# Performance work log

Hardware: AMD Instinct MI355X
Metric: run time of the kernel (lower is better)

## Reference

```python
import jax, jax.numpy as jnp
import numpy as np

EPS = 1e-5

def _layernorm(x, g, b):
    # LayerNorm over last dim (head_dim), eps=1e-5 like nn.LayerNorm
    mu = jnp.mean(x, axis=-1, keepdims=True)
    var = jnp.mean(jnp.square(x - mu), axis=-1, keepdims=True)
    return (x - mu) * jax.lax.rsqrt(var + EPS) * g + b

def _rotate_half(x):
    d = x.shape[-1] // 2
    return jnp.concatenate([-x[..., d:], x[..., :d]], axis=-1)

def _apply_rotary(x, cos, sin):
    # x: [B,S,H,D]; cos/sin: [S,D] broadcast over batch and heads
    c = cos[None, :, None, :]
    s = sin[None, :, None, :]
    return x * c + _rotate_half(x) * s

def setup_inputs() -> dict:
    key = jax.random.key(0)
    ks = jax.random.split(key, 16)
    B, S, Dm = 2, 1024, 2048
    H, Hkv, Dh = 16, 4, 128
    f = lambda k, shp: (jax.random.normal(k, shp, dtype=jnp.float32) * 0.02)
    return {
        "hidden_states": jax.random.normal(ks[0], (B, S, Dm), dtype=jnp.float32),
        "cos": jax.random.uniform(ks[1], (S, Dh), dtype=jnp.float32),
        "sin": jax.random.uniform(ks[2], (S, Dh), dtype=jnp.float32),
        "Wq": f(ks[3], (H * Dh, Dm)),   "bq": jnp.zeros((H * Dh,), jnp.float32),
        "Wk": f(ks[4], (Hkv * Dh, Dm)), "bk": jnp.zeros((Hkv * Dh,), jnp.float32),
        "Wv": f(ks[5], (Hkv * Dh, Dm)), "bv": jnp.zeros((Hkv * Dh,), jnp.float32),
        "Wo": f(ks[6], (Dm, H * Dh)),   "bo": jnp.zeros((Dm,), jnp.float32),
        "qn_g": jnp.ones((Dh,), jnp.float32), "qn_b": jnp.zeros((Dh,), jnp.float32),
        "kn_g": jnp.ones((Dh,), jnp.float32), "kn_b": jnp.zeros((Dh,), jnp.float32),
        "cu_seqlens": jnp.array([0, S, 2 * S], dtype=jnp.int32),
        "max_s": 1024,
    }

def reference(hidden_states, cos, sin, Wq, bq, Wk, bk, Wv, bv, Wo, bo,
              qn_g, qn_b, kn_g, kn_b, cu_seqlens, max_s):
    B, S, Dm = hidden_states.shape
    Dh = qn_g.shape[0]
    H = Wq.shape[0] // Dh
    Hkv = Wk.shape[0] // Dh
    scale = 1.0 / jnp.sqrt(jnp.float32(Dh))

    q = (hidden_states @ Wq.T + bq).reshape(B, S, H, Dh)
    k = (hidden_states @ Wk.T + bk).reshape(B, S, Hkv, Dh)
    v = (hidden_states @ Wv.T + bv).reshape(B, S, Hkv, Dh)

    q = _apply_rotary(_layernorm(q, qn_g, qn_b), cos, sin)
    k = _apply_rotary(_layernorm(k, kn_g, kn_b), cos, sin)

    # GQA: repeat_interleave kv heads to match q heads
    n_rep = H // Hkv
    if n_rep > 1:
        k = jnp.repeat(k, n_rep, axis=2)
        v = jnp.repeat(v, n_rep, axis=2)

    # scores: [B,H,S,S]
    scores = jnp.einsum('bqhd,bkhd->bhqk', q, k) * scale
    causal = jnp.tril(jnp.ones((S, S), dtype=bool))
    scores = jnp.where(causal[None, None], scores, jnp.finfo(scores.dtype).min)
    weights = jax.nn.softmax(scores, axis=-1)
    out = jnp.einsum('bhqk,bkhd->bqhd', weights, v).reshape(B, S, H * Dh)
    return out @ Wo.T + bo
```

## Files before the change

kernel.cpp:

```cpp
#include <hip/hip_runtime.h>
#include <cmath>

typedef __attribute__((ext_vector_type(8))) short bf16x8;
typedef __attribute__((ext_vector_type(4))) short s16x4;
typedef __attribute__((ext_vector_type(4))) float f32x4;

#define MFMA_BF16 __builtin_amdgcn_mfma_f32_16x16x32_bf16

__device__ __forceinline__ float bf2f(short s) {
    unsigned u = ((unsigned)(unsigned short)s) << 16;
    return __builtin_bit_cast(float, u);
}
__device__ __forceinline__ short f2bf(float f) {
    unsigned u = __builtin_bit_cast(unsigned, f);
    u += 0x7fffu + ((u >> 16) & 1u);
    return (short)(u >> 16);
}

__device__ __forceinline__ void gl_lds16(const short* gp, short* lp) {
    __builtin_amdgcn_global_load_lds(
        (const __attribute__((address_space(1))) unsigned int*)gp,
        (__attribute__((address_space(3))) unsigned int*)lp, 16, 0, 0);
}

__global__ __launch_bounds__(256) void cvt5(
    const float* s0, short* d0, int n0,
    const float* s1, short* d1, int n1,
    const float* s2, short* d2, int n2,
    const float* s3, short* d3, int n3,
    const float* s4, short* d4, int n4)
{
    long long i = (long long)blockIdx.x * 1024 + threadIdx.x * 4;
    const float* s; short* d;
    if      (i < n0)                  { s = s0; d = d0; }
    else if ((i -= n0) < n1)          { s = s1; d = d1; }
    else if ((i -= n1) < n2)          { s = s2; d = d2; }
    else if ((i -= n2) < n3)          { s = s3; d = d3; }
    else      { i -= n3;                s = s4; d = d4; }
    float4 v = *(const float4*)(s + i);
    s16x4 o;
    o[0] = f2bf(v.x); o[1] = f2bf(v.y); o[2] = f2bf(v.z); o[3] = f2bf(v.w);
    *(s16x4*)(d + i) = o;
}

template <int MODE>
__global__ __launch_bounds__(256) void gemm_t(
    const short* __restrict__ A, const short* __restrict__ W,
    const float* __restrict__ bq, const float* __restrict__ bk,
    const float* __restrict__ bv,
    short* __restrict__ qo, short* __restrict__ ko, short* __restrict__ vo,
    float* __restrict__ fo,
    int M, int K, int S, int Hkv, int Nq, int Nkv, int N)
{
    __shared__ __align__(16) short As[2][8 * 512];
    __shared__ __align__(16) short Bs[2][4 * 512];

    const int w    = threadIdx.x >> 6;
    const int lane = threadIdx.x & 63;
    const int l15  = lane & 15;
    const int quad = lane >> 4;
    const int wy   = w >> 1;
    const int wx   = w & 1;

    unsigned gx = gridDim.x, gy = gridDim.y;
    unsigned bx = blockIdx.x, by = blockIdx.y;
    if ((gx & 3) == 0 && (gy & 1) == 0) {
        unsigned lin = by * gx + bx;
        unsigned xcd = lin & 7, idx = lin >> 3;
        unsigned n   = gx >> 2;
        bx = (xcd & 3) * n + idx % n;
        by = (xcd >> 2) * (gy >> 1) + idx / n;
    }
    const int m0 = by * 128;
    const int n0 = bx * 64;

    const short* Ab = A + (size_t)m0 * K;
    const short* Wb = W + (size_t)n0 * K;

    const int srow = lane >> 2;
    const int scol = ((lane & 3) ^ ((srow >> 1) & 3)) * 8;
    auto stage = [&](int buf, int kofs) {
#pragma unroll
        for (int i = 0; i < 2; i++) {
            const int c = 2 * w + i;
            gl_lds16(Ab + (size_t)(c * 16 + srow) * K + kofs + scol,
                     As[buf] + c * 512 + lane * 8);
        }
        gl_lds16(Wb + (size_t)(w * 16 + srow) * K + kofs + scol,
                 Bs[buf] + w * 512 + lane * 8);
    };

    f32x4 acc[4][2];
#pragma unroll
    for (int i = 0; i < 4; i++)
#pragma unroll
        for (int j = 0; j < 2; j++) acc[i][j] = f32x4{0.f, 0.f, 0.f, 0.f};

    const int ridx = (l15 * 4 + (quad ^ ((l15 >> 1) & 3))) * 8;
    const int nk = K / 32;
    stage(0, 0);
    __syncthreads();

    for (int kt = 0; kt < nk; kt++) {
        const int cur = kt & 1;
        if (kt + 1 < nk) stage(cur ^ 1, (kt + 1) * 32);

        bf16x8 af[4], bfr[2];
#pragma unroll
        for (int i = 0; i < 4; i++)
            af[i] = *(const bf16x8*)(As[cur] + (wy * 4 + i) * 512 + ridx);
#pragma unroll
        for (int j = 0; j < 2; j++)
            bfr[j] = *(const bf16x8*)(Bs[cur] + (wx * 2 + j) * 512 + ridx);
#pragma unroll
        for (int i = 0; i < 4; i++)
#pragma unroll
            for (int j = 0; j < 2; j++)
                acc[i][j] = MFMA_BF16(af[i], bfr[j], acc[i][j], 0, 0, 0);
        __syncthreads();
    }

#pragma unroll
    for (int i = 0; i < 4; i++) {
#pragma unroll
        for (int j = 0; j < 2; j++) {
            const int col = n0 + wx * 32 + j * 16 + l15;
#pragma unroll
            for (int r = 0; r < 4; r++) {
                const int row = m0 + wy * 64 + i * 16 + quad * 4 + r;
                float v = acc[i][j][r];
                if constexpr (MODE == 0) {
                    if (col < Nq) {
                        qo[(size_t)row * Nq + col] = f2bf(v + bq[col]);
                    } else if (col < Nq + Nkv) {
                        int cn = col - Nq;
                        ko[(size_t)row * Nkv + cn] = f2bf(v + bk[cn]);
                    } else {
                        int cn = col - Nq - Nkv;
                        int b  = row / S, s = row - b * S;
                        int hk = cn >> 7, dh = cn & 127;
                        vo[(size_t)((b * Hkv + hk) * 128 + dh) * S + s] = f2bf(v + bv[cn]);
                    }
                } else {
                    fo[(size_t)row * N + col] = v + bq[col];
                }
            }
        }
    }
}

__global__ __launch_bounds__(256) void ln_rope2(
    const short* __restrict__ Xq, short* __restrict__ Yq,
    const short* __restrict__ Xk, short* __restrict__ Yk,
    const float* __restrict__ qg, const float* __restrict__ qbe,
    const float* __restrict__ kg, const float* __restrict__ kbe,
    const float* __restrict__ cosp, const float* __restrict__ sinp,
    int H, int Hkv, int S, int nq)
{
    int gw = blockIdx.x * 4 + (threadIdx.x >> 6);
    const int lane = threadIdx.x & 63;
    const short* X; short* Y; const float* g; const float* bt; int Hc;
    if (gw < nq) { X = Xq; Y = Yq; g = qg; bt = qbe; Hc = H; }
    else { gw -= nq; X = Xk; Y = Yk; g = kg; bt = kbe; Hc = Hkv; }

    const int h  = gw % Hc;
    const int rs = gw / Hc;
    const int b  = rs / S;
    const int s  = rs - b * S;

    const short* x = X + ((size_t)rs * Hc + h) * 128;
    float x0 = bf2f(x[lane]), x1 = bf2f(x[lane + 64]);

    float sum = x0 + x1;
    float sq  = x0 * x0 + x1 * x1;
#pragma unroll
    for (int off = 32; off > 0; off >>= 1) {
        sum += __shfl_xor(sum, off, 64);
        sq  += __shfl_xor(sq, off, 64);
    }
    float mu  = sum * (1.f / 128.f);
    float var = sq * (1.f / 128.f) - mu * mu;
    float rinv = rsqrtf(var + 1e-5f);

    float y0 = (x0 - mu) * rinv * g[lane]      + bt[lane];
    float y1 = (x1 - mu) * rinv * g[lane + 64] + bt[lane + 64];

    float c0 = cosp[(size_t)s * 128 + lane];
    float c1 = cosp[(size_t)s * 128 + lane + 64];
    float s0 = sinp[(size_t)s * 128 + lane];
    float s1 = sinp[(size_t)s * 128 + lane + 64];

    float o0 = y0 * c0 - y1 * s0;
    float o1 = y1 * c1 + y0 * s1;

    short* yp = Y + ((size_t)(b * Hc + h) * S + s) * 128;
    yp[lane]      = f2bf(o0);
    yp[lane + 64] = f2bf(o1);
}

__global__ __launch_bounds__(256, 2) void attn(
    const short* __restrict__ Q, const short* __restrict__ Kt,
    const short* __restrict__ Vt, short* __restrict__ O,
    int S, int H, int Hkv, int nrep, float scale)
{
    __shared__ __align__(16) short Ks[2][16 * 512];
    __shared__ __align__(16) short Vs[2][16 * 512];
    __shared__ __align__(16) short P[4][16][72];

    const int w    = threadIdx.x >> 6;
    const int lane = threadIdx.x & 63;
    const int l15  = lane & 15;
    const int quad = lane >> 4;
    const int bh   = blockIdx.x;
    const int h    = bh % H;
    const int b    = bh / H;
    const int nyt  = gridDim.y;
    const int y    = blockIdx.y;
    const int qblk = (y < (nyt >> 1)) ? (nyt - 1 - y) : (y - (nyt >> 1));
    const int hk   = h / nrep;
    const int m0   = qblk * 64 + w * 16;
    const int qpos = m0 + l15;

    const short* qb = Q  + (size_t)(b * H + h) * S * 128;
    const short* kb = Kt + (size_t)(b * Hkv + hk) * S * 128;
    const short* vb = Vt + (size_t)(b * Hkv + hk) * 128 * S;

    auto stage = [&](int buf, int j0) {
#pragma unroll
        for (int i = 0; i < 8; i++) {
            if (w < 2) {
                const int s = w * 8 + i;
                const int t = s >> 2, c = s & 3;
                gl_lds16(kb + (size_t)(j0 + t * 16 + l15) * 128 + c * 32 + quad * 8,
                         Ks[buf] + s * 512 + lane * 8);
            } else {
                const int u = (w - 2) * 8 + i;
                const int c = u >> 1, hf = u & 1;
                gl_lds16(vb + (size_t)(c * 16 + l15) * S + j0 + hf * 32 + quad * 8,
                         Vs[buf] + u * 512 + lane * 8);
            }
        }
    };

    bf16x8 qf[4];
#pragma unroll
    for (int c = 0; c < 4; c++)
        qf[c] = *(const bf16x8*)(qb + (size_t)(m0 + l15) * 128 + c * 32 + quad * 8);

    f32x4 of[8];
#pragma unroll
    for (int c = 0; c < 8; c++) of[c] = f32x4{0.f, 0.f, 0.f, 0.f};
    float m_s = -1e30f, l_s = 0.f;
    const float c2 = scale * 1.44269504f;

    const int nkt = qblk + 1;
    stage(0, 0);
    __syncthreads();

    for (int kt = 0; kt < nkt; kt++) {
        const int cur = kt & 1;
        if (kt + 1 < nkt) stage(cur ^ 1, (kt + 1) * 64);

        const short* Kb = Ks[cur];
        const short* Vb = Vs[cur];
        const int j0 = kt * 64;

        f32x4 sc[4];
#pragma unroll
        for (int t = 0; t < 4; t++) sc[t] = f32x4{0.f, 0.f, 0.f, 0.f};
#pragma unroll
        for (int c = 0; c < 4; c++)
#pragma unroll
            for (int t = 0; t < 4; t++) {
                bf16x8 kf = *(const bf16x8*)(Kb + (t * 4 + c) * 512 + lane * 8);
                sc[t] = MFMA_BF16(kf, qf[c], sc[t], 0, 0, 0);
            }

        float v[4][4];
        float mx = -1e30f;
#pragma unroll
        for (int t = 0; t < 4; t++)
#pragma unroll
            for (int r = 0; r < 4; r++) {
                float s_ = sc[t][r];
                if (j0 + t * 16 + quad * 4 + r > qpos) s_ = -1e30f;
                v[t][r] = s_;
                mx = fmaxf(mx, s_);
            }
        mx = fmaxf(mx, __shfl_xor(mx, 16, 64));
        mx = fmaxf(mx, __shfl_xor(mx, 32, 64));
        float mnew  = fmaxf(m_s, mx);
        float mc    = mnew * c2;
        float alpha = exp2f(m_s * c2 - mc);
        float sum = 0.f;
        float p[4][4];
#pragma unroll
        for (int t = 0; t < 4; t++)
#pragma unroll
            for (int r = 0; r < 4; r++) {
                p[t][r] = exp2f(__builtin_fmaf(v[t][r], c2, -mc));
                sum += p[t][r];
            }
        sum += __shfl_xor(sum, 16, 64);
        sum += __shfl_xor(sum, 32, 64);
        l_s = l_s * alpha + sum;
        m_s = mnew;

#pragma unroll
        for (int c = 0; c < 8; c++) {
            f32x4 t = of[c];
            t[0] *= alpha; t[1] *= alpha; t[2] *= alpha; t[3] *= alpha;
            of[c] = t;
        }

#pragma unroll
        for (int t = 0; t < 4; t++) {
            s16x4 pk;
#pragma unroll
            for (int r = 0; r < 4; r++) pk[r] = f2bf(p[t][r]);
            *(s16x4*)(&P[w][l15][t * 16 + quad * 4]) = pk;
        }
        bf16x8 pb0 = *(const bf16x8*)(&P[w][l15][quad * 8]);
        bf16x8 pb1 = *(const bf16x8*)(&P[w][l15][32 + quad * 8]);

#pragma unroll
        for (int c = 0; c < 8; c++) {
            bf16x8 vf0 = *(const bf16x8*)(Vb + (c * 2 + 0) * 512 + lane * 8);
            bf16x8 vf1 = *(const bf16x8*)(Vb + (c * 2 + 1) * 512 + lane * 8);
            of[c] = MFMA_BF16(vf0, pb0, of[c], 0, 0, 0);
            of[c] = MFMA_BF16(vf1, pb1, of[c], 0, 0, 0);
        }
        __syncthreads();
    }

    const int HDh = H * 128;
    const float rinv = 1.0f / l_s;
    short* orow = O + ((size_t)b * S + qpos) * HDh + h * 128;
#pragma unroll
    for (int c = 0; c < 8; c++) {
        s16x4 ov;
#pragma unroll
        for (int r = 0; r < 4; r++) ov[r] = f2bf(of[c][r] * rinv);
        *(s16x4*)(orow + c * 16 + quad * 4) = ov;
    }
}

extern "C" void kernel_launch(void* const* d_in, const int* in_sizes, int n_in,
                              void* d_out, int out_size, void* d_ws, size_t ws_size,
                              hipStream_t stream) {
    const float* hs   = (const float*)d_in[0];
    const float* cosp = (const float*)d_in[1];
    const float* sinp = (const float*)d_in[2];
    const float* Wq   = (const float*)d_in[3];
    const float* bq   = (const float*)d_in[4];
    const float* Wk   = (const float*)d_in[5];
    const float* bk   = (const float*)d_in[6];
    const float* Wv   = (const float*)d_in[7];
    const float* bv   = (const float*)d_in[8];
    const float* Wo   = (const float*)d_in[9];
    const float* bo   = (const float*)d_in[10];
    const float* qg   = (const float*)d_in[11];
    const float* qb_  = (const float*)d_in[12];
    const float* kg   = (const float*)d_in[13];
    const float* kb_  = (const float*)d_in[14];

    const int Dh    = in_sizes[11];
    const int Dm    = in_sizes[10];
    const int HDh   = in_sizes[4];
    const int H     = HDh / Dh;
    const int HkvDh = in_sizes[6];
    const int Hkv   = HkvDh / Dh;
    const int S     = in_sizes[1] / Dh;
    const int B     = in_sizes[0] / (S * Dm);
    const int M     = B * S;
    const int nrep  = H / Hkv;

    char* ws = (char*)d_ws;
    short* hsb  = (short*)ws;  ws += (size_t)M * Dm      * 2;
    short* Wqb  = (short*)ws;  ws += (size_t)HDh * Dm    * 2;
    short* Wkb  = (short*)ws;  ws += (size_t)HkvDh * Dm  * 2;
    short* Wvb  = (short*)ws;  ws += (size_t)HkvDh * Dm  * 2;
    short* Wob  = (short*)ws;  ws += (size_t)Dm * HDh    * 2;
    short* qg16 = (short*)ws;  ws += (size_t)M * HDh     * 2;
    short* kg16 = (short*)ws;  ws += (size_t)M * HkvDh   * 2;
    short* qbuf = (short*)ws;  ws += (size_t)M * HDh     * 2;
    short* kbuf = (short*)ws;  ws += (size_t)M * HkvDh   * 2;
    short* vbuf = (short*)ws;  ws += (size_t)M * HkvDh   * 2;
    short* abuf = qg16;

    dim3 blk(256);
    const int n0 = M * Dm, n1 = HDh * Dm, n2 = HkvDh * Dm, n3 = HkvDh * Dm, n4 = Dm * HDh;
    cvt5<<<dim3((n0 + n1 + n2 + n3 + n4) / 1024), blk, 0, stream>>>(
        hs, hsb, n0, Wq, Wqb, n1, Wk, Wkb, n2, Wv, Wvb, n3, Wo, Wob, n4);

    const int Ntot = HDh + 2 * HkvDh;
    gemm_t<0><<<dim3(Ntot / 64, M / 128), blk, 0, stream>>>(
        hsb, Wqb, bq, bk, bv, qg16, kg16, vbuf, nullptr,
        M, Dm, S, Hkv, HDh, HkvDh, Ntot);

    const int nq = M * H;
    ln_rope2<<<dim3((nq + M * Hkv) / 4), blk, 0, stream>>>(
        qg16, qbuf, kg16, kbuf, qg, qb_, kg, kb_, cosp, sinp, H, Hkv, S, nq);

    const float scale = 1.0f / sqrtf((float)Dh);
    attn<<<dim3(H * B, S / 64), blk, 0, stream>>>(qbuf, kbuf, vbuf, abuf, S, H, Hkv, nrep, scale);

    gemm_t<1><<<dim3(Dm / 64, M / 128), blk, 0, stream>>>(
        abuf, Wob, bo, nullptr, nullptr, nullptr, nullptr, nullptr, (float*)d_out,
        M, HDh, S, Hkv, Dm, 0, Dm);
}
```

Baseline: 252.6 us.

## Load GEMM A fragments directly into registers and deepen K step to 64

```diff
diff --git a/kernel.cpp b/kernel.cpp
--- a/kernel.cpp
+++ b/kernel.cpp
@@ -52,8 +52,7 @@
     float* __restrict__ fo,
     int M, int K, int S, int Hkv, int Nq, int Nkv, int N)
 {
-    __shared__ __align__(16) short As[2][8 * 512];
-    __shared__ __align__(16) short Bs[2][4 * 512];
+    __shared__ __align__(16) short Bs[2][2 * 4 * 512];
 
     const int w    = threadIdx.x >> 6;
     const int lane = threadIdx.x & 63;
@@ -74,22 +73,24 @@
     const int m0 = by * 128;
     const int n0 = bx * 64;
 
-    const short* Ab = A + (size_t)m0 * K;
     const short* Wb = W + (size_t)n0 * K;
+    const short* Arow = A + (size_t)(m0 + wy * 64 + l15) * K + quad * 8;
 
     const int srow = lane >> 2;
     const int scol = ((lane & 3) ^ ((srow >> 1) & 3)) * 8;
-    auto stage = [&](int buf, int kofs) {
-#pragma unroll
-        for (int i = 0; i < 2; i++) {
-            const int c = 2 * w + i;
-            gl_lds16(Ab + (size_t)(c * 16 + srow) * K + kofs + scol,
-                     As[buf] + c * 512 + lane * 8);
-        }
-        gl_lds16(Wb + (size_t)(w * 16 + srow) * K + kofs + scol,
-                 Bs[buf] + w * 512 + lane * 8);
+    auto stageW = [&](int buf, int kofs) {
+#pragma unroll
+        for (int h2 = 0; h2 < 2; h2++)
+            gl_lds16(Wb + (size_t)(w * 16 + srow) * K + kofs + h2 * 32 + scol,
+                     Bs[buf] + h2 * 2048 + w * 512 + lane * 8);
     };
 
+    bf16x8 afc[4], afn[4];
+#define LOAD_A(dst, k)                                                        \
+    _Pragma("unroll")                                                         \
+    for (int i_ = 0; i_ < 4; i_++)                                            \
+        dst[i_] = *(const bf16x8*)(Arow + (size_t)i_ * 16 * K + (k));
+
     f32x4 acc[4][2];
 #pragma unroll
     for (int i = 0; i < 4; i++)
@@ -97,28 +98,46 @@
         for (int j = 0; j < 2; j++) acc[i][j] = f32x4{0.f, 0.f, 0.f, 0.f};
 
     const int ridx = (l15 * 4 + (quad ^ ((l15 >> 1) & 3))) * 8;
-    const int nk = K / 32;
-    stage(0, 0);
+    const int nk = K / 64;
+
+    LOAD_A(afc, 0);
+    stageW(0, 0);
+    LOAD_A(afn, 32);
     __syncthreads();
 
     for (int kt = 0; kt < nk; kt++) {
         const int cur = kt & 1;
-        if (kt + 1 < nk) stage(cur ^ 1, (kt + 1) * 32);
-
-        bf16x8 af[4], bfr[2];
-#pragma unroll
-        for (int i = 0; i < 4; i++)
-            af[i] = *(const bf16x8*)(As[cur] + (wy * 4 + i) * 512 + ridx);
-#pragma unroll
-        for (int j = 0; j < 2; j++)
-            bfr[j] = *(const bf16x8*)(Bs[cur] + (wx * 2 + j) * 512 + ridx);
-#pragma unroll
-        for (int i = 0; i < 4; i++)
+        if (kt + 1 < nk) stageW(cur ^ 1, (kt + 1) * 64);
+
+        {
+            bf16x8 bfr[2];
 #pragma unroll
             for (int j = 0; j < 2; j++)
-                acc[i][j] = MFMA_BF16(af[i], bfr[j], acc[i][j], 0, 0, 0);
+                bfr[j] = *(const bf16x8*)(Bs[cur] + (wx * 2 + j) * 512 + ridx);
+#pragma unroll
+            for (int i = 0; i < 4; i++)
+#pragma unroll
+                for (int j = 0; j < 2; j++)
+                    acc[i][j] = MFMA_BF16(afc[i], bfr[j], acc[i][j], 0, 0, 0);
+        }
+        if (kt + 1 < nk) { LOAD_A(afc, (kt + 1) * 64); }
+
+        {
+            bf16x8 bfr[2];
+#pragma unroll
+            for (int j = 0; j < 2; j++)
+                bfr[j] = *(const bf16x8*)(Bs[cur] + 2048 + (wx * 2 + j) * 512 + ridx);
+#pragma unroll
+            for (int i = 0; i < 4; i++)
+#pragma unroll
+                for (int j = 0; j < 2; j++)
+                    acc[i][j] = MFMA_BF16(afn[i], bfr[j], acc[i][j], 0, 0, 0);
+        }
+        if (kt + 1 < nk) { LOAD_A(afn, (kt + 1) * 64 + 32); }
+
         __syncthreads();
     }
+#undef LOAD_A
 
 #pragma unroll
     for (int i = 0; i < 4; i++) {
```

After: 333.8 us. 32.2% more time.

## Split K across two warp groups in GEMM with LDS reduction

Applied to the files above, without the earlier changes.

```diff
diff --git a/kernel.cpp b/kernel.cpp
--- a/kernel.cpp
+++ b/kernel.cpp
@@ -44,7 +44,7 @@
 }
 
 template <int MODE>
-__global__ __launch_bounds__(256) void gemm_t(
+__global__ __launch_bounds__(512) void gemm_t(
     const short* __restrict__ A, const short* __restrict__ W,
     const float* __restrict__ bq, const float* __restrict__ bk,
     const float* __restrict__ bv,
@@ -52,14 +52,15 @@
     float* __restrict__ fo,
     int M, int K, int S, int Hkv, int Nq, int Nkv, int N)
 {
-    __shared__ __align__(16) short As[2][8 * 512];
-    __shared__ __align__(16) short Bs[2][4 * 512];
+    __shared__ __align__(16) short As[2][2 * 8 * 512];
+    __shared__ __align__(16) short Bs[2][2 * 4 * 512];
 
     const int w    = threadIdx.x >> 6;
     const int lane = threadIdx.x & 63;
     const int l15  = lane & 15;
     const int quad = lane >> 4;
-    const int wy   = w >> 1;
+    const int kg   = w >> 2;
+    const int wy   = (w >> 1) & 1;
     const int wx   = w & 1;
 
     unsigned gx = gridDim.x, gy = gridDim.y;
@@ -82,12 +83,16 @@
     auto stage = [&](int buf, int kofs) {
 #pragma unroll
         for (int i = 0; i < 2; i++) {
-            const int c = 2 * w + i;
-            gl_lds16(Ab + (size_t)(c * 16 + srow) * K + kofs + scol,
-                     As[buf] + c * 512 + lane * 8);
-        }
-        gl_lds16(Wb + (size_t)(w * 16 + srow) * K + kofs + scol,
-                 Bs[buf] + w * 512 + lane * 8);
+            const int a  = 2 * w + i;
+            const int h2 = a >> 3, c = a & 7;
+            gl_lds16(Ab + (size_t)(c * 16 + srow) * K + kofs + h2 * 32 + scol,
+                     As[buf] + a * 512 + lane * 8);
+        }
+        {
+            const int h2 = w >> 2, c4 = w & 3;
+            gl_lds16(Wb + (size_t)(c4 * 16 + srow) * K + kofs + h2 * 32 + scol,
+                     Bs[buf] + w * 512 + lane * 8);
+        }
     };
 
     f32x4 acc[4][2];
@@ -97,21 +102,21 @@
         for (int j = 0; j < 2; j++) acc[i][j] = f32x4{0.f, 0.f, 0.f, 0.f};
 
     const int ridx = (l15 * 4 + (quad ^ ((l15 >> 1) & 3))) * 8;
-    const int nk = K / 32;
+    const int nk = K / 64;
     stage(0, 0);
     __syncthreads();
 
     for (int kt = 0; kt < nk; kt++) {
         const int cur = kt & 1;
-        if (kt + 1 < nk) stage(cur ^ 1, (kt + 1) * 32);
+        if (kt + 1 < nk) stage(cur ^ 1, (kt + 1) * 64);
 
         bf16x8 af[4], bfr[2];
 #pragma unroll
         for (int i = 0; i < 4; i++)
-            af[i] = *(const bf16x8*)(As[cur] + (wy * 4 + i) * 512 + ridx);
+            af[i] = *(const bf16x8*)(As[cur] + kg * 4096 + (wy * 4 + i) * 512 + ridx);
 #pragma unroll
         for (int j = 0; j < 2; j++)
-            bfr[j] = *(const bf16x8*)(Bs[cur] + (wx * 2 + j) * 512 + ridx);
+            bfr[j] = *(const bf16x8*)(Bs[cur] + kg * 2048 + (wx * 2 + j) * 512 + ridx);
 #pragma unroll
         for (int i = 0; i < 4; i++)
 #pragma unroll
@@ -120,29 +125,49 @@
         __syncthreads();
     }
 
-#pragma unroll
-    for (int i = 0; i < 4; i++) {
-#pragma unroll
-        for (int j = 0; j < 2; j++) {
-            const int col = n0 + wx * 32 + j * 16 + l15;
-#pragma unroll
-            for (int r = 0; r < 4; r++) {
-                const int row = m0 + wy * 64 + i * 16 + quad * 4 + r;
-                float v = acc[i][j][r];
-                if constexpr (MODE == 0) {
-                    if (col < Nq) {
-                        qo[(size_t)row * Nq + col] = f2bf(v + bq[col]);
-                    } else if (col < Nq + Nkv) {
-                        int cn = col - Nq;
-                        ko[(size_t)row * Nkv + cn] = f2bf(v + bk[cn]);
+    float* scratch = (float*)&As[0][0];
+    if (w >= 4) {
+#pragma unroll
+        for (int i = 0; i < 4; i++)
+#pragma unroll
+            for (int j = 0; j < 2; j++)
+                *(f32x4*)(scratch + (w - 4) * 2048 + (i * 2 + j) * 256 + lane * 4) = acc[i][j];
+    }
+    __syncthreads();
+    if (w < 4) {
+#pragma unroll
+        for (int i = 0; i < 4; i++)
+#pragma unroll
+            for (int j = 0; j < 2; j++) {
+                f32x4 p = *(const f32x4*)(scratch + w * 2048 + (i * 2 + j) * 256 + lane * 4);
+                acc[i][j][0] += p[0]; acc[i][j][1] += p[1];
+                acc[i][j][2] += p[2]; acc[i][j][3] += p[3];
+            }
+
+#pragma unroll
+        for (int i = 0; i < 4; i++) {
+#pragma unroll
+            for (int j = 0; j < 2; j++) {
+                const int col = n0 + wx * 32 + j * 16 + l15;
+#pragma unroll
+                for (int r = 0; r < 4; r++) {
+                    const int row = m0 + wy * 64 + i * 16 + quad * 4 + r;
+                    float v = acc[i][j][r];
+                    if constexpr (MODE == 0) {
+                        if (col < Nq) {
+                            qo[(size_t)row * Nq + col] = f2bf(v + bq[col]);
+                        } else if (col < Nq + Nkv) {
+                            int cn = col - Nq;
+                            ko[(size_t)row * Nkv + cn] = f2bf(v + bk[cn]);
+                        } else {
+                            int cn = col - Nq - Nkv;
+                            int b  = row / S, s = row - b * S;
+                            int hk = cn >> 7, dh = cn & 127;
+                            vo[(size_t)((b * Hkv + hk) * 128 + dh) * S + s] = f2bf(v + bv[cn]);
+                        }
                     } else {
-                        int cn = col - Nq - Nkv;
-                        int b  = row / S, s = row - b * S;
-                        int hk = cn >> 7, dh = cn & 127;
-                        vo[(size_t)((b * Hkv + hk) * 128 + dh) * S + s] = f2bf(v + bv[cn]);
+                        fo[(size_t)row * N + col] = v + bq[col];
                     }
-                } else {
-                    fo[(size_t)row * N + col] = v + bq[col];
                 }
             }
         }
@@ -388,13 +413,13 @@
     short* vbuf = (short*)ws;  ws += (size_t)M * HkvDh   * 2;
     short* abuf = qg16;
 
-    dim3 blk(256);
+    dim3 blk(256), blk512(512);
     const int n0 = M * Dm, n1 = HDh * Dm, n2 = HkvDh * Dm, n3 = HkvDh * Dm, n4 = Dm * HDh;
     cvt5<<<dim3((n0 + n1 + n2 + n3 + n4) / 1024), blk, 0, stream>>>(
         hs, hsb, n0, Wq, Wqb, n1, Wk, Wkb, n2, Wv, Wvb, n3, Wo, Wob, n4);
 
     const int Ntot = HDh + 2 * HkvDh;
-    gemm_t<0><<<dim3(Ntot / 64, M / 128), blk, 0, stream>>>(
+    gemm_t<0><<<dim3(Ntot / 64, M / 128), blk512, 0, stream>>>(
         hsb, Wqb, bq, bk, bv, qg16, kg16, vbuf, nullptr,
         M, Dm, S, Hkv, HDh, HkvDh, Ntot);
 
@@ -405,7 +430,7 @@
     const float scale = 1.0f / sqrtf((float)Dh);
     attn<<<dim3(H * B, S / 64), blk, 0, stream>>>(qbuf, kbuf, vbuf, abuf, S, H, Hkv, nrep, scale);
 
-    gemm_t<1><<<dim3(Dm / 64, M / 128), blk, 0, stream>>>(
+    gemm_t<1><<<dim3(Dm / 64, M / 128), blk512, 0, stream>>>(
         abuf, Wob, bo, nullptr, nullptr, nullptr, nullptr, nullptr, (float*)d_out,
         M, HDh, S, Hkv, Dm, 0, Dm);
 }
```

After: 249.5 us. About the same (-1.2%).
